# Kernel tuning notes

Measured on AMD Instinct MI355X. Metric: run time of the kernel, lower is better.

## Reference

```python
import jax, jax.numpy as jnp
import numpy as np
import math

EMBED_DIM = 1024
NUM_HEADS = 16
D_K = EMBED_DIM // NUM_HEADS  # 64 qubits per head
BATCH, SEQ = 4, 2048


def setup_inputs() -> dict:
    key = jax.random.key(0)
    k_x, k_th, k_w, k_b = jax.random.split(key, 4)
    x = jax.random.normal(k_x, (BATCH, SEQ, EMBED_DIM), dtype=jnp.float32)
    # trainable RX angle per head per qubit (tq.RX has one param each)
    theta = jax.random.normal(k_th, (NUM_HEADS, D_K), dtype=jnp.float32)
    # out_linear
    lim = 1.0 / math.sqrt(EMBED_DIM)
    w_out = jax.random.uniform(k_w, (EMBED_DIM, EMBED_DIM), jnp.float32, -lim, lim)
    b_out = jax.random.uniform(k_b, (EMBED_DIM,), jnp.float32, -lim, lim)
    return {"x": x, "theta": theta, "w_out": w_out, "b_out": b_out}


def reference(x, theta, w_out, b_out):
    B, S, E = x.shape
    H, d_k = theta.shape
    # Quantum head: RX(x_i) then RX(theta_i) on |0>, measure PauliZ ->
    # <Z_i> = cos(x_i + theta_i). No entangling gates in the code path.
    ang = x.reshape(B, S, H, d_k) + theta  # broadcast [H,d_k]
    qkv = jnp.cos(ang).transpose(0, 2, 1, 3)  # [B,H,S,d_k]; Q == K == V
    scale = 1.0 / math.sqrt(d_k)
    scores = jnp.einsum('bhqd,bhkd->bhqk', qkv, qkv) * scale
    attn = jax.nn.softmax(scores, axis=-1)  # dropout is identity in eval
    out = jnp.einsum('bhqk,bhkd->bhqd', attn, qkv)
    out = out.transpose(0, 2, 1, 3).reshape(B, S, E)
    return out @ w_out.T + b_out
```

## Files before the change

kernel.cpp:

```cpp
#include <hip/hip_runtime.h>


#define B_  4
#define S_  2048
#define H_  16
#define D_  64
#define E_  1024
#define EXP2_SCALE 0.18033688011112043f

typedef unsigned short u16;
typedef unsigned int u32;
typedef __attribute__((ext_vector_type(8))) short short8;
typedef __attribute__((ext_vector_type(4))) float floatx4;

static __device__ __forceinline__ float bf2f(u16 v) {
    return __uint_as_float(((unsigned)v) << 16);
}
static __device__ __forceinline__ u16 f2bf(float f) {
    unsigned u = __float_as_uint(f);
    return (u16)((u + 0x7FFFu + ((u >> 16) & 1u)) >> 16);
}
static __device__ __forceinline__ u32 pack_bf16_trunc(float lo, float hi) {
    return __builtin_amdgcn_perm(__float_as_uint(hi), __float_as_uint(lo), 0x07060302u);
}
static __device__ __forceinline__ short8 scale8(short8 v) {
    short8 o;
#pragma unroll
    for (int i = 0; i < 8; i++)
        o[i] = (short)f2bf(bf2f((u16)v[i]) * EXP2_SCALE);
    return o;
}

__global__ __launch_bounds__(256) void prep_kernel(const float* __restrict__ x,
                                                   const float* __restrict__ theta,
                                                   const float* __restrict__ W,
                                                   u16* __restrict__ qkv,
                                                   u16* __restrict__ qkvT,
                                                   u16* __restrict__ Wb) {
    __shared__ __align__(16) u16 TQ[64][72];
    int blk = blockIdx.x;
    int tid = threadIdx.x;
    if (blk >= 2048) {
        int i = ((blk - 2048) * 256 + tid) * 4;
        float4 w = *(const float4*)(W + i);
        ushort4 o;
        o.x = f2bf(w.x); o.y = f2bf(w.y); o.z = f2bf(w.z); o.w = f2bf(w.w);
        *(ushort4*)(Wb + i) = o;
        return;
    }
    int stile = blk & 31;
    int bh    = blk >> 5;
    int b     = bh >> 4;
    int h     = bh & 15;
    int i     = tid >> 2;
    int d0    = (tid & 3) << 4;
    int s0    = stile << 6;
    int s     = s0 + i;

    const float* xp = x + ((size_t)(b * S_ + s)) * E_ + h * D_ + d0;
    const float* tp = theta + h * D_ + d0;

    u16 ov[16];
#pragma unroll
    for (int j = 0; j < 16; j += 4) {
        float4 xv = *(const float4*)(xp + j);
        float4 tv = *(const float4*)(tp + j);
        ov[j]     = f2bf(__cosf(xv.x + tv.x));
        ov[j + 1] = f2bf(__cosf(xv.y + tv.y));
        ov[j + 2] = f2bf(__cosf(xv.z + tv.z));
        ov[j + 3] = f2bf(__cosf(xv.w + tv.w));
    }

    u16* qp = qkv + ((size_t)bh * S_ + s) * D_ + d0;
    *(uint4*)qp       = *(uint4*)&ov[0];
    *(uint4*)(qp + 8) = *(uint4*)&ov[8];

#pragma unroll
    for (int j = 0; j < 16; j++) TQ[d0 + j][i] = ov[j];
    __syncthreads();

    int d  = tid >> 2;
    int j0 = (tid & 3) << 4;
    u16 tmp[16];
#pragma unroll
    for (int j = 0; j < 16; j++) tmp[j] = TQ[d][j0 + j];
    u16* qtp = qkvT + ((size_t)bh * D_ + d) * S_ + s0 + j0;
    *(uint4*)qtp       = *(uint4*)&tmp[0];
    *(uint4*)(qtp + 8) = *(uint4*)&tmp[8];
}

__global__ __launch_bounds__(256, 4) void attn_kernel(const u16* __restrict__ qkv,
                                                      const u16* __restrict__ qkvT,
                                                      u16* __restrict__ aout) {
    int blk  = blockIdx.x;
    int qt   = blk & 15;
    int bh   = blk >> 4;
    int b    = bh >> 4;
    int h    = bh & 15;
    int tid  = threadIdx.x;
    int wave = tid >> 6;
    int lane = tid & 63;
    int lq   = lane & 15;
    int lg   = lane >> 4;
    int r    = tid >> 2;
    int c0   = (tid & 3) << 4;

    __shared__ __align__(16) u16 Kt[64][72];
    __shared__ __align__(16) u16 Vt[64][72];
    __shared__ __align__(16) u16 Pb[4][32][72];

    const u16* base  = qkv  + (size_t)bh * S_ * D_;
    const u16* baseT = qkvT + (size_t)bh * D_ * S_;
    int s0 = qt * 128;

    short8 bq[2][2];
#pragma unroll
    for (int rf = 0; rf < 2; rf++) {
        const u16* qrow = base + (size_t)(s0 + wave * 32 + rf * 16 + lq) * D_ + lg * 8;
        bq[rf][0] = scale8(*(const short8*)qrow);
        bq[rf][1] = scale8(*(const short8*)(qrow + 32));
    }

    floatx4 oacc[2][4] = {{{0,0,0,0},{0,0,0,0},{0,0,0,0},{0,0,0,0}},
                          {{0,0,0,0},{0,0,0,0},{0,0,0,0},{0,0,0,0}}};
    float lsum[2] = {0.f, 0.f};

    for (int kt = 0; kt < S_ / 64; kt++) {
        __syncthreads();
        {
            const u16* p = base + (size_t)(kt * 64 + r) * D_ + c0;
            *(uint4*)&Kt[r][c0]     = *(const uint4*)p;
            *(uint4*)&Kt[r][c0 + 8] = *(const uint4*)(p + 8);
            const u16* p2 = baseT + (size_t)r * S_ + kt * 64 + c0;
            *(uint4*)&Vt[r][c0]     = *(const uint4*)p2;
            *(uint4*)&Vt[r][c0 + 8] = *(const uint4*)(p2 + 8);
        }
        __syncthreads();

        floatx4 sc[2][4];
#pragma unroll
        for (int t = 0; t < 4; t++) {
            short8 a0 = *(short8*)&Kt[t * 16 + lq][lg * 8];
            short8 a1 = *(short8*)&Kt[t * 16 + lq][32 + lg * 8];
#pragma unroll
            for (int rf = 0; rf < 2; rf++) {
                floatx4 acc = {0, 0, 0, 0};
                acc = __builtin_amdgcn_mfma_f32_16x16x32_bf16(a0, bq[rf][0], acc, 0, 0, 0);
                sc[rf][t] = __builtin_amdgcn_mfma_f32_16x16x32_bf16(a1, bq[rf][1], acc, 0, 0, 0);
            }
        }

#pragma unroll
        for (int rf = 0; rf < 2; rf++) {
#pragma unroll
            for (int t = 0; t < 4; t++) {
                float p0 = __builtin_amdgcn_exp2f(sc[rf][t][0]);
                float p1 = __builtin_amdgcn_exp2f(sc[rf][t][1]);
                float p2 = __builtin_amdgcn_exp2f(sc[rf][t][2]);
                float p3 = __builtin_amdgcn_exp2f(sc[rf][t][3]);
                lsum[rf] += (p0 + p1) + (p2 + p3);
                uint2 w;
                w.x = pack_bf16_trunc(p0, p1);
                w.y = pack_bf16_trunc(p2, p3);
                *(uint2*)&Pb[wave][rf * 16 + lq][t * 16 + lg * 4] = w;
            }
        }

        asm volatile("s_waitcnt lgkmcnt(0)" ::: "memory");

        short8 bp[2][2];
#pragma unroll
        for (int rf = 0; rf < 2; rf++) {
            bp[rf][0] = *(short8*)&Pb[wave][rf * 16 + lq][lg * 8];
            bp[rf][1] = *(short8*)&Pb[wave][rf * 16 + lq][32 + lg * 8];
        }
#pragma unroll
        for (int t = 0; t < 4; t++) {
            short8 av0 = *(short8*)&Vt[t * 16 + lq][lg * 8];
            short8 av1 = *(short8*)&Vt[t * 16 + lq][32 + lg * 8];
#pragma unroll
            for (int rf = 0; rf < 2; rf++) {
                oacc[rf][t] = __builtin_amdgcn_mfma_f32_16x16x32_bf16(av0, bp[rf][0], oacc[rf][t], 0, 0, 0);
                oacc[rf][t] = __builtin_amdgcn_mfma_f32_16x16x32_bf16(av1, bp[rf][1], oacc[rf][t], 0, 0, 0);
            }
        }
    }

#pragma unroll
    for (int rf = 0; rf < 2; rf++) {
        lsum[rf] += __shfl_xor(lsum[rf], 16);
        lsum[rf] += __shfl_xor(lsum[rf], 32);
    }
#pragma unroll
    for (int rf = 0; rf < 2; rf++) {
        float inv = 1.0f / fmaxf(lsum[rf], 1e-20f);
        int srow = s0 + wave * 32 + rf * 16 + lq;
        u16* arow = aout + ((size_t)(b * S_ + srow)) * E_ + h * D_;
#pragma unroll
        for (int t = 0; t < 4; t++)
#pragma unroll
            for (int rr = 0; rr < 4; rr++)
                arow[t * 16 + lg * 4 + rr] = f2bf(oacc[rf][t][rr] * inv);
    }
}

__global__ __launch_bounds__(256) void proj_kernel(const u16* __restrict__ A,
                                                   const u16* __restrict__ Wb,
                                                   const float* __restrict__ bias,
                                                   float* __restrict__ out) {
    int m0   = blockIdx.x * 128;
    int n0   = blockIdx.y * 128;
    int tid  = threadIdx.x;
    int wave = tid >> 6;
    int wm   = wave >> 1;
    int wn   = wave & 1;
    int lane = tid & 63;
    int lq   = lane & 15;
    int lg   = lane >> 4;
    int r    = tid >> 1;
    int c0   = (tid & 1) * 32;

    __shared__ __align__(16) u16 As[128][72];
    __shared__ __align__(16) u16 Bs[128][72];

    floatx4 acc[4][4];
#pragma unroll
    for (int i = 0; i < 4; i++)
#pragma unroll
        for (int j = 0; j < 4; j++) acc[i][j] = (floatx4){0, 0, 0, 0};

    for (int kc = 0; kc < E_; kc += 64) {
        __syncthreads();
        const u16* pa = A + (size_t)(m0 + r) * E_ + kc + c0;
        const u16* pw = Wb + (size_t)(n0 + r) * E_ + kc + c0;
#pragma unroll
        for (int j = 0; j < 4; j++) {
            *(uint4*)&As[r][c0 + j * 8] = *(const uint4*)(pa + j * 8);
            *(uint4*)&Bs[r][c0 + j * 8] = *(const uint4*)(pw + j * 8);
        }
        __syncthreads();

#pragma unroll
        for (int c = 0; c < 2; c++) {
            short8 af[4], bf[4];
#pragma unroll
            for (int i = 0; i < 4; i++)
                af[i] = *(short8*)&As[wm * 64 + i * 16 + lq][c * 32 + lg * 8];
#pragma unroll
            for (int j = 0; j < 4; j++)
                bf[j] = *(short8*)&Bs[wn * 64 + j * 16 + lq][c * 32 + lg * 8];
#pragma unroll
            for (int i = 0; i < 4; i++)
#pragma unroll
                for (int j = 0; j < 4; j++)
                    acc[i][j] = __builtin_amdgcn_mfma_f32_16x16x32_bf16(af[i], bf[j], acc[i][j], 0, 0, 0);
        }
    }

#pragma unroll
    for (int j = 0; j < 4; j++) {
        int nidx = n0 + wn * 64 + j * 16 + lq;
        float bv = bias[nidx];
#pragma unroll
        for (int i = 0; i < 4; i++) {
#pragma unroll
            for (int rr = 0; rr < 4; rr++) {
                int row = m0 + wm * 64 + i * 16 + lg * 4 + rr;
                out[(size_t)row * E_ + nidx] = acc[i][j][rr] + bv;
            }
        }
    }
}

extern "C" void kernel_launch(void* const* d_in, const int* in_sizes, int n_in,
                              void* d_out, int out_size, void* d_ws, size_t ws_size,
                              hipStream_t stream) {
    const float* x     = (const float*)d_in[0];
    const float* theta = (const float*)d_in[1];
    const float* w_out = (const float*)d_in[2];
    const float* b_out = (const float*)d_in[3];
    float* out = (float*)d_out;

    char* ws = (char*)d_ws;
    const size_t QKV_BYTES = (size_t)B_ * H_ * S_ * D_ * sizeof(u16);
    u16* qkv  = (u16*)ws;
    u16* qkvT = (u16*)(ws + QKV_BYTES);
    u16* aout = (u16*)(ws + 2 * QKV_BYTES);
    u16* wbf  = (u16*)ws;
    u16* wbf_safe = (u16*)(ws + 3 * QKV_BYTES);

    prep_kernel<<<3072, 256, 0, stream>>>(x, theta, w_out, qkv, qkvT, wbf_safe);
    attn_kernel<<<(B_ * H_) * (S_ / 128), 256, 0, stream>>>(qkv, qkvT, aout);
    dim3 pg(B_ * S_ / 128, E_ / 128);
    proj_kernel<<<pg, 256, 0, stream>>>(aout, wbf_safe, b_out, out);
    (void)wbf;
}
```

Baseline: 204.6 us.

## Register-prefetch next K/V tile, XOR-swizzle LDS, setprio around MFMA, remap blocks

Measured after the change: 401.8 us. 1.96x slower.

```diff
diff --git a/kernel.cpp b/kernel.cpp
--- a/kernel.cpp
+++ b/kernel.cpp
@@ -30,6 +30,8 @@
         o[i] = (short)f2bf(bf2f((u16)v[i]) * EXP2_SCALE);
     return o;
 }
+
+#define KSWZ(r, c) ((((r)) << 6) + (((c) ^ ((((r)) & 7) << 3))))
 
 __global__ __launch_bounds__(256) void prep_kernel(const float* __restrict__ x,
                                                    const float* __restrict__ theta,
@@ -89,10 +91,11 @@
     *(uint4*)(qtp + 8) = *(uint4*)&tmp[8];
 }
 
-__global__ __launch_bounds__(256, 4) void attn_kernel(const u16* __restrict__ qkv,
+__global__ __launch_bounds__(256, 5) void attn_kernel(const u16* __restrict__ qkv,
                                                       const u16* __restrict__ qkvT,
                                                       u16* __restrict__ aout) {
-    int blk  = blockIdx.x;
+    int blk0 = blockIdx.x;
+    int blk  = (blk0 & 7) * 128 + (blk0 >> 3);
     int qt   = blk & 15;
     int bh   = blk >> 4;
     int b    = bh >> 4;
@@ -105,9 +108,9 @@
     int r    = tid >> 2;
     int c0   = (tid & 3) << 4;
 
-    __shared__ __align__(16) u16 Kt[64][72];
-    __shared__ __align__(16) u16 Vt[64][72];
-    __shared__ __align__(16) u16 Pb[4][32][72];
+    __shared__ __align__(16) u16 Kt[64 * 64];
+    __shared__ __align__(16) u16 Vt[64 * 64];
+    __shared__ __align__(16) u16 Pb[4][32 * 64];
 
     const u16* base  = qkv  + (size_t)bh * S_ * D_;
     const u16* baseT = qkvT + (size_t)bh * D_ * S_;
@@ -125,23 +128,33 @@
                           {{0,0,0,0},{0,0,0,0},{0,0,0,0},{0,0,0,0}}};
     float lsum[2] = {0.f, 0.f};
 
+    {
+        const u16* p = base + (size_t)r * D_ + c0;
+        *(uint4*)&Kt[KSWZ(r, c0)]     = *(const uint4*)p;
+        *(uint4*)&Kt[KSWZ(r, c0 + 8)] = *(const uint4*)(p + 8);
+        const u16* p2 = baseT + (size_t)r * S_ + c0;
+        *(uint4*)&Vt[KSWZ(r, c0)]     = *(const uint4*)p2;
+        *(uint4*)&Vt[KSWZ(r, c0 + 8)] = *(const uint4*)(p2 + 8);
+    }
+    __syncthreads();
+
     for (int kt = 0; kt < S_ / 64; kt++) {
-        __syncthreads();
-        {
-            const u16* p = base + (size_t)(kt * 64 + r) * D_ + c0;
-            *(uint4*)&Kt[r][c0]     = *(const uint4*)p;
-            *(uint4*)&Kt[r][c0 + 8] = *(const uint4*)(p + 8);
-            const u16* p2 = baseT + (size_t)r * S_ + kt * 64 + c0;
-            *(uint4*)&Vt[r][c0]     = *(const uint4*)p2;
-            *(uint4*)&Vt[r][c0 + 8] = *(const uint4*)(p2 + 8);
-        }
-        __syncthreads();
+        uint4 nk0, nk1, nv0, nv1;
+        if (kt < S_ / 64 - 1) {
+            const u16* p = base + (size_t)((kt + 1) * 64 + r) * D_ + c0;
+            nk0 = *(const uint4*)p;
+            nk1 = *(const uint4*)(p + 8);
+            const u16* p2 = baseT + (size_t)r * S_ + (kt + 1) * 64 + c0;
+            nv0 = *(const uint4*)p2;
+            nv1 = *(const uint4*)(p2 + 8);
+        }
 
         floatx4 sc[2][4];
+        __builtin_amdgcn_s_setprio(1);
 #pragma unroll
         for (int t = 0; t < 4; t++) {
-            short8 a0 = *(short8*)&Kt[t * 16 + lq][lg * 8];
-            short8 a1 = *(short8*)&Kt[t * 16 + lq][32 + lg * 8];
+            short8 a0 = *(short8*)&Kt[KSWZ(t * 16 + lq, lg * 8)];
+            short8 a1 = *(short8*)&Kt[KSWZ(t * 16 + lq, 32 + lg * 8)];
 #pragma unroll
             for (int rf = 0; rf < 2; rf++) {
                 floatx4 acc = {0, 0, 0, 0};
@@ -149,6 +162,7 @@
                 sc[rf][t] = __builtin_amdgcn_mfma_f32_16x16x32_bf16(a1, bq[rf][1], acc, 0, 0, 0);
             }
         }
+        __builtin_amdgcn_s_setprio(0);
 
 #pragma unroll
         for (int rf = 0; rf < 2; rf++) {
@@ -162,7 +176,7 @@
                 uint2 w;
                 w.x = pack_bf16_trunc(p0, p1);
                 w.y = pack_bf16_trunc(p2, p3);
-                *(uint2*)&Pb[wave][rf * 16 + lq][t * 16 + lg * 4] = w;
+                *(uint2*)&Pb[wave][KSWZ(rf * 16 + lq, t * 16 + lg * 4)] = w;
             }
         }
 
@@ -171,18 +185,29 @@
         short8 bp[2][2];
 #pragma unroll
         for (int rf = 0; rf < 2; rf++) {
-            bp[rf][0] = *(short8*)&Pb[wave][rf * 16 + lq][lg * 8];
-            bp[rf][1] = *(short8*)&Pb[wave][rf * 16 + lq][32 + lg * 8];
-        }
+            bp[rf][0] = *(short8*)&Pb[wave][KSWZ(rf * 16 + lq, lg * 8)];
+            bp[rf][1] = *(short8*)&Pb[wave][KSWZ(rf * 16 + lq, 32 + lg * 8)];
+        }
+        __builtin_amdgcn_s_setprio(1);
 #pragma unroll
         for (int t = 0; t < 4; t++) {
-            short8 av0 = *(short8*)&Vt[t * 16 + lq][lg * 8];
-            short8 av1 = *(short8*)&Vt[t * 16 + lq][32 + lg * 8];
+            short8 av0 = *(short8*)&Vt[KSWZ(t * 16 + lq, lg * 8)];
+            short8 av1 = *(short8*)&Vt[KSWZ(t * 16 + lq, 32 + lg * 8)];
 #pragma unroll
             for (int rf = 0; rf < 2; rf++) {
                 oacc[rf][t] = __builtin_amdgcn_mfma_f32_16x16x32_bf16(av0, bp[rf][0], oacc[rf][t], 0, 0, 0);
                 oacc[rf][t] = __builtin_amdgcn_mfma_f32_16x16x32_bf16(av1, bp[rf][1], oacc[rf][t], 0, 0, 0);
             }
+        }
+        __builtin_amdgcn_s_setprio(0);
+
+        __syncthreads();
+        if (kt < S_ / 64 - 1) {
+            *(uint4*)&Kt[KSWZ(r, c0)]     = nk0;
+            *(uint4*)&Kt[KSWZ(r, c0 + 8)] = nk1;
+            *(uint4*)&Vt[KSWZ(r, c0)]     = nv0;
+            *(uint4*)&Vt[KSWZ(r, c0 + 8)] = nv1;
+            __syncthreads();
         }
     }
 
@@ -286,12 +311,10 @@
     u16* qkv  = (u16*)ws;
     u16* qkvT = (u16*)(ws + QKV_BYTES);
     u16* aout = (u16*)(ws + 2 * QKV_BYTES);
-    u16* wbf  = (u16*)ws;
     u16* wbf_safe = (u16*)(ws + 3 * QKV_BYTES);
 
     prep_kernel<<<3072, 256, 0, stream>>>(x, theta, w_out, qkv, qkvT, wbf_safe);
     attn_kernel<<<(B_ * H_) * (S_ / 128), 256, 0, stream>>>(qkv, qkvT, aout);
     dim3 pg(B_ * S_ / 128, E_ / 128);
     proj_kernel<<<pg, 256, 0, stream>>>(aout, wbf_safe, b_out, out);
-    (void)wbf;
-}
+}
```
